# Kernel tuning notes

Measured on AMD Instinct MI355X. Metric: run time of the kernel, lower is better.

## Reference

```python
import jax, jax.numpy as jnp
import numpy as np

N = 8192      # nodes (overlap.shape[0])
NNZ = 262144  # nonzeros in overlap coo (avg degree 32)
E = 32768     # query edges
PSI1 = 64     # psi_1_dim
PSI2 = 64     # psi_2_dim


def _lin(k, fan_in, fan_out):
    return jax.random.normal(k, (fan_in, fan_out), jnp.float32) / np.float32(np.sqrt(fan_in))


def setup_inputs() -> dict:
    key = jax.random.key(0)
    ks = jax.random.split(key, 12)
    row = jax.random.randint(ks[0], (NNZ,), 0, N)
    col = jax.random.randint(ks[1], (NNZ,), 0, N)
    values = jax.random.uniform(ks[2], (NNZ,), dtype=jnp.float32)
    # dense form of the same coo matrix (overlap.todense())
    adj = jnp.zeros((N, N), jnp.float32).at[row, col].add(values)
    src_nodes = jax.random.randint(ks[3], (E,), 0, N)
    return {
        "col": col,
        "values": values,
        "adj": adj,
        "src_nodes": src_nodes,
        "w1e": _lin(ks[4], 1, PSI1), "b1e": jnp.zeros((PSI1,), jnp.float32),
        "w2e": _lin(ks[5], PSI1, 1), "b2e": jnp.zeros((1,), jnp.float32),
        "w1n": _lin(ks[6], 1, PSI2), "b1n": jnp.zeros((PSI2,), jnp.float32),
        "w2n": _lin(ks[7], PSI2, 1), "b2n": jnp.zeros((1,), jnp.float32),
    }


def _mlp(x, w1, b1, w2, b2):
    # Linear(1, psi) -> ReLU -> Linear(psi, 1), applied per scalar
    return jax.nn.relu(x @ w1 + b1) @ w2 + b2


def reference(col, values, adj, src_nodes, w1e, b1e, w2e, b2e, w1n, b1n, w2n, b2n):
    # f_edge on each nonzero overlap value: [NNZ,1]
    edge_feat = _mlp(values[:, None], w1e, b1e, w2e, b2e)
    # scatter_add by column index -> per-node aggregate [N,1]
    agg = jax.ops.segment_sum(edge_feat, col, num_segments=N)
    # f_node -> structural score per node [N]
    struct = _mlp(agg, w1n, b1n, w2n, b2n)[:, 0]
    # gather dense adjacency rows for edge endpoints [E,N]
    src_rows = adj[src_nodes]
    struct_src = src_rows * struct
    struct_dst = src_rows * struct  # faithful to original: dst also uses src_nodes
    # row-wise dot product -> [E,1]
    return jnp.einsum('ij,ij->i', struct_src, struct_dst)[:, None]
```

## Files before the change

### kernel.cpp

```cpp
#include <hip/hip_runtime.h>

#define N_NODES 8192
#define NNZV    262144
#define E_EDGES 32768
#define PSI     64

__global__ void edge_mlp_scatter(const int* __restrict__ col,
                                 const float* __restrict__ values,
                                 const float* __restrict__ w1e,
                                 const float* __restrict__ b1e,
                                 const float* __restrict__ w2e,
                                 const float* __restrict__ b2e,
                                 float* __restrict__ agg) {
    __shared__ float sw1[PSI], sb1[PSI], sw2[PSI];
    int t = threadIdx.x;
    if (t < PSI) { sw1[t] = w1e[t]; sb1[t] = b1e[t]; sw2[t] = w2e[t]; }
    __syncthreads();
    int i = blockIdx.x * blockDim.x + t;
    if (i >= NNZV) return;
    float v = values[i];
    float f = b2e[0];
    #pragma unroll
    for (int j = 0; j < PSI; ++j) {
        float h = fmaf(v, sw1[j], sb1[j]);
        f += (h > 0.f ? h * sw2[j] : 0.f);
    }
    atomicAdd(&agg[col[i]], f);
}

__global__ void node_mlp_sq(const float* __restrict__ agg,
                            const float* __restrict__ w1n,
                            const float* __restrict__ b1n,
                            const float* __restrict__ w2n,
                            const float* __restrict__ b2n,
                            float* __restrict__ s2) {
    __shared__ float sw1[PSI], sb1[PSI], sw2[PSI];
    int t = threadIdx.x;
    if (t < PSI) { sw1[t] = w1n[t]; sb1[t] = b1n[t]; sw2[t] = w2n[t]; }
    __syncthreads();
    int n = blockIdx.x * blockDim.x + t;
    if (n >= N_NODES) return;
    float a = agg[n];
    float s = b2n[0];
    #pragma unroll
    for (int j = 0; j < PSI; ++j) {
        float h = fmaf(a, sw1[j], sb1[j]);
        s += (h > 0.f ? h * sw2[j] : 0.f);
    }
    s2[n] = s * s;
}

__global__ __launch_bounds__(256) void row_dot(const float* __restrict__ adj,
                                               const float* __restrict__ s2,
                                               float* __restrict__ r) {
    int row = blockIdx.x;
    const float4* arow = (const float4*)(adj + (size_t)row * N_NODES);
    const float4* s4   = (const float4*)s2;
    float acc = 0.f;
    #pragma unroll
    for (int j = 0; j < (N_NODES / 4) / 256; ++j) {
        int idx = threadIdx.x + j * 256;
        float4 a = arow[idx];
        float4 s = s4[idx];
        acc += a.x * a.x * s.x + a.y * a.y * s.y + a.z * a.z * s.z + a.w * a.w * s.w;
    }
    #pragma unroll
    for (int off = 32; off > 0; off >>= 1) acc += __shfl_down(acc, off, 64);
    __shared__ float part[4];
    int lane = threadIdx.x & 63, wid = threadIdx.x >> 6;
    if (lane == 0) part[wid] = acc;
    __syncthreads();
    if (threadIdx.x == 0) r[row] = part[0] + part[1] + part[2] + part[3];
}

__global__ void gather_out(const int* __restrict__ src,
                           const float* __restrict__ r,
                           float* __restrict__ out) {
    int e = blockIdx.x * blockDim.x + threadIdx.x;
    if (e < E_EDGES) out[e] = r[src[e]];
}

extern "C" void kernel_launch(void* const* d_in, const int* in_sizes, int n_in,
                              void* d_out, int out_size, void* d_ws, size_t ws_size,
                              hipStream_t stream) {
    const int*   col       = (const int*)d_in[0];
    const float* values    = (const float*)d_in[1];
    const float* adj       = (const float*)d_in[2];
    const int*   src_nodes = (const int*)d_in[3];
    const float* w1e = (const float*)d_in[4];
    const float* b1e = (const float*)d_in[5];
    const float* w2e = (const float*)d_in[6];
    const float* b2e = (const float*)d_in[7];
    const float* w1n = (const float*)d_in[8];
    const float* b1n = (const float*)d_in[9];
    const float* w2n = (const float*)d_in[10];
    const float* b2n = (const float*)d_in[11];
    float* out = (float*)d_out;

    float* agg = (float*)d_ws;
    float* s2  = agg + N_NODES;
    float* r   = s2 + N_NODES;

    hipMemsetAsync(agg, 0, N_NODES * sizeof(float), stream);

    edge_mlp_scatter<<<NNZV / 256, 256, 0, stream>>>(col, values, w1e, b1e, w2e, b2e, agg);
    node_mlp_sq<<<N_NODES / 256, 256, 0, stream>>>(agg, w1n, b1n, w2n, b2n, s2);
    row_dot<<<N_NODES, 256, 0, stream>>>(adj, s2, r);
    gather_out<<<E_EDGES / 256, 256, 0, stream>>>(src_nodes, r, out);
}
```

Before: 67.45 us.

## Fuse all stages into one cooperative grid-synced kernel with nontemporal loads

Replaces the memset and four separate launches with a single cooperative kernel that uses grid.sync between the edge MLP scatter, node MLP, row-dot and gather phases. Each block handles eight adjacency rows using nontemporal vector loads. This removes launch gaps and inter-kernel bubbles. In exchange it adds grid-wide barriers, and the fixed 1024-block grid may reduce memory-level parallelism in the bandwidth-bound row-dot phase. It falls back to the old path if co-residency is not possible.

```diff
diff --git a/kernel.cpp b/kernel.cpp
--- a/kernel.cpp
+++ b/kernel.cpp
@@ -1,9 +1,101 @@
 #include <hip/hip_runtime.h>
+#include <hip/hip_cooperative_groups.h>
+
+namespace cg = cooperative_groups;
 
 #define N_NODES 8192
 #define NNZV    262144
 #define E_EDGES 32768
 #define PSI     64
+#define NTHR    256
+#define NBLK    1024
+#define ROWS    8
+
+typedef float f32x4 __attribute__((ext_vector_type(4)));
+
+__global__ __launch_bounds__(NTHR, 4) void fused_all(
+    const int* __restrict__ col, const float* __restrict__ values,
+    const float* __restrict__ adj, const int* __restrict__ src,
+    const float* __restrict__ w1e, const float* __restrict__ b1e,
+    const float* __restrict__ w2e, const float* __restrict__ b2e,
+    const float* __restrict__ w1n, const float* __restrict__ b1n,
+    const float* __restrict__ w2n, const float* __restrict__ b2n,
+    float* __restrict__ agg, float* __restrict__ s2g,
+    float* __restrict__ r, float* __restrict__ out)
+{
+    cg::grid_group grid = cg::this_grid();
+    __shared__ float wbuf[3 * PSI];
+    __shared__ float redbuf[4][ROWS];
+
+    const int t = threadIdx.x;
+    const int bid = blockIdx.x;
+    const int gtid = bid * NTHR + t;
+
+    for (int n = gtid; n < N_NODES; n += NBLK * NTHR) agg[n] = 0.f;
+    if (t < PSI) { wbuf[t] = w1e[t]; wbuf[PSI + t] = b1e[t]; wbuf[2 * PSI + t] = w2e[t]; }
+    grid.sync();
+
+    {
+        const int i = gtid;
+        float v = values[i];
+        float f = b2e[0];
+        #pragma unroll
+        for (int j = 0; j < PSI; ++j) {
+            float h = fmaf(v, wbuf[j], wbuf[PSI + j]);
+            f += (h > 0.f ? h * wbuf[2 * PSI + j] : 0.f);
+        }
+        atomicAdd(&agg[col[i]], f);
+    }
+    grid.sync();
+
+    if (t < PSI) { wbuf[t] = w1n[t]; wbuf[PSI + t] = b1n[t]; wbuf[2 * PSI + t] = w2n[t]; }
+    __syncthreads();
+
+    for (int n = gtid; n < N_NODES; n += NBLK * NTHR) {
+        float a = agg[n];
+        float s = b2n[0];
+        #pragma unroll
+        for (int j = 0; j < PSI; ++j) {
+            float h = fmaf(a, wbuf[j], wbuf[PSI + j]);
+            s += (h > 0.f ? h * wbuf[2 * PSI + j] : 0.f);
+        }
+        s2g[n] = s * s;
+    }
+    grid.sync();
+
+    const f32x4* s4 = (const f32x4*)s2g;
+    float acc[ROWS];
+    #pragma unroll
+    for (int i = 0; i < ROWS; ++i) acc[i] = 0.f;
+
+    #pragma unroll
+    for (int i = 0; i < ROWS; ++i) {
+        const int row = bid * ROWS + i;
+        const f32x4* arow = (const f32x4*)(adj + (size_t)row * N_NODES);
+        #pragma unroll
+        for (int j = 0; j < (N_NODES / 4) / NTHR; ++j) {
+            int idx = t + j * NTHR;
+            f32x4 a = __builtin_nontemporal_load(&arow[idx]);
+            f32x4 s = s4[idx];
+            f32x4 p = a * a * s;
+            acc[i] += p.x + p.y + p.z + p.w;
+        }
+    }
+
+    const int lane = t & 63, wid = t >> 6;
+    #pragma unroll
+    for (int i = 0; i < ROWS; ++i) {
+        float a = acc[i];
+        #pragma unroll
+        for (int off = 32; off > 0; off >>= 1) a += __shfl_down(a, off, 64);
+        if (lane == 0) redbuf[wid][i] = a;
+    }
+    __syncthreads();
+    if (t < ROWS) r[bid * ROWS + t] = redbuf[0][t] + redbuf[1][t] + redbuf[2][t] + redbuf[3][t];
+    grid.sync();
+
+    for (int e = gtid; e < E_EDGES; e += NBLK * NTHR) out[e] = r[src[e]];
+}
 
 __global__ void edge_mlp_scatter(const int* __restrict__ col,
                                  const float* __restrict__ values,
@@ -50,19 +142,20 @@
     s2[n] = s * s;
 }
 
-__global__ __launch_bounds__(256) void row_dot(const float* __restrict__ adj,
-                                               const float* __restrict__ s2,
-                                               float* __restrict__ r) {
+__global__ __launch_bounds__(NTHR) void row_dot(const float* __restrict__ adj,
+                                                const float* __restrict__ s2,
+                                                float* __restrict__ r) {
     int row = blockIdx.x;
-    const float4* arow = (const float4*)(adj + (size_t)row * N_NODES);
-    const float4* s4   = (const float4*)s2;
+    const f32x4* arow = (const f32x4*)(adj + (size_t)row * N_NODES);
+    const f32x4* s4   = (const f32x4*)s2;
     float acc = 0.f;
     #pragma unroll
-    for (int j = 0; j < (N_NODES / 4) / 256; ++j) {
-        int idx = threadIdx.x + j * 256;
-        float4 a = arow[idx];
-        float4 s = s4[idx];
-        acc += a.x * a.x * s.x + a.y * a.y * s.y + a.z * a.z * s.z + a.w * a.w * s.w;
+    for (int j = 0; j < (N_NODES / 4) / NTHR; ++j) {
+        int idx = threadIdx.x + j * NTHR;
+        f32x4 a = __builtin_nontemporal_load(&arow[idx]);
+        f32x4 s = s4[idx];
+        f32x4 p = a * a * s;
+        acc += p.x + p.y + p.z + p.w;
     }
     #pragma unroll
     for (int off = 32; off > 0; off >>= 1) acc += __shfl_down(acc, off, 64);
@@ -95,16 +188,32 @@
     const float* b1n = (const float*)d_in[9];
     const float* w2n = (const float*)d_in[10];
     const float* b2n = (const float*)d_in[11];
-    float* out = (float*)d_out;
+    float* outp = (float*)d_out;
 
     float* agg = (float*)d_ws;
-    float* s2  = agg + N_NODES;
-    float* r   = s2 + N_NODES;
+    float* s2g = agg + N_NODES;
+    float* r   = s2g + N_NODES;
+
+    int maxBlkPerCU = 0, numCU = 0;
+    bool coop_ok = false;
+    if (hipOccupancyMaxActiveBlocksPerMultiprocessor(&maxBlkPerCU, fused_all, NTHR, 0) == hipSuccess &&
+        hipDeviceGetAttribute(&numCU, hipDeviceAttributeMultiprocessorCount, 0) == hipSuccess) {
+        coop_ok = ((long)maxBlkPerCU * numCU >= NBLK);
+    }
+
+    if (coop_ok) {
+        void* args[] = { &col, &values, &adj, &src_nodes,
+                         &w1e, &b1e, &w2e, &b2e, &w1n, &b1n, &w2n, &b2n,
+                         &agg, &s2g, &r, &outp };
+        if (hipLaunchCooperativeKernel((void*)fused_all, dim3(NBLK), dim3(NTHR),
+                                       args, 0, stream) == hipSuccess) {
+            return;
+        }
+    }
 
     hipMemsetAsync(agg, 0, N_NODES * sizeof(float), stream);
-
-    edge_mlp_scatter<<<NNZV / 256, 256, 0, stream>>>(col, values, w1e, b1e, w2e, b2e, agg);
-    node_mlp_sq<<<N_NODES / 256, 256, 0, stream>>>(agg, w1n, b1n, w2n, b2n, s2);
-    row_dot<<<N_NODES, 256, 0, stream>>>(adj, s2, r);
-    gather_out<<<E_EDGES / 256, 256, 0, stream>>>(src_nodes, r, out);
-}
+    edge_mlp_scatter<<<NNZV / NTHR, NTHR, 0, stream>>>(col, values, w1e, b1e, w2e, b2e, agg);
+    node_mlp_sq<<<N_NODES / NTHR, NTHR, 0, stream>>>(agg, w1n, b1n, w2n, b2n, s2g);
+    row_dot<<<N_NODES, NTHR, 0, stream>>>(adj, s2g, r);
+    gather_out<<<E_EDGES / NTHR, NTHR, 0, stream>>>(src_nodes, r, outp);
+}
```

Result: slower. 71.26 us (+5.6%).
